# Optimization experiments

Hardware: AMD Instinct MI355X
Metric: run time of the kernel (lower is better)

Reference implementation:

```python
import jax, jax.numpy as jnp
import numpy as np

N = 1048576
NUM_POINTS = 9
L = 3
EPS = 1e-6
GMM_EPS = 1e-6  # diagonal regularizer used by the GaussianMixture fit


def _det2(m):
    return m[..., 0, 0] * m[..., 1, 1] - m[..., 0, 1] * m[..., 1, 0]


def _inv2(m, det):
    # closed-form 2x2 inverse via adjugate
    adj = jnp.stack([
        jnp.stack([m[..., 1, 1], -m[..., 0, 1]], axis=-1),
        jnp.stack([-m[..., 1, 0], m[..., 0, 0]], axis=-1),
    ], axis=-2)
    return adj / det[..., None, None]


def setup_inputs() -> dict:
    key = jax.random.key(0)
    k1, k2, k3, k4, k5, k6 = jax.random.split(key, 6)
    # ground-truth rotated rectangles -> 4 corners (N, 4, 2)
    center = jax.random.uniform(k1, (N, 2), jnp.float32, 0.0, 512.0)
    w = jax.random.uniform(k2, (N,), jnp.float32, 10.0, 60.0)
    h = jax.random.uniform(k3, (N,), jnp.float32, 10.0, 60.0)
    th = jax.random.uniform(k4, (N,), jnp.float32, 0.0, np.pi)
    c, s = jnp.cos(th), jnp.sin(th)
    # local corners ordered so edge 0->1 is the width axis, 1->2 the height axis
    lx = jnp.stack([-w, w, w, -w], axis=1) * 0.5  # (N,4)
    ly = jnp.stack([-h, -h, h, h], axis=1) * 0.5
    gx = c[:, None] * lx - s[:, None] * ly + center[:, 0:1]
    gy = s[:, None] * lx + c[:, None] * ly + center[:, 1:2]
    target = jnp.stack([gx, gy], axis=-1).astype(jnp.float32)  # (N,4,2)
    # predicted convex points scattered around the box center
    pred = center[:, None, :] + 5.0 * jax.random.normal(k5, (N, NUM_POINTS, 2), jnp.float32)
    return {"pred": pred, "target": target}


def reference(pred, target):
    pred = pred.reshape(-1, NUM_POINTS, 2)
    target = target.reshape(-1, 4, 2)
    # --- GMM fit (1 component) == closed-form MLE Gaussian ---
    p_mu = pred.mean(axis=1)                       # (N,2)
    xm = pred - p_mu[:, None, :]                   # (N,9,2)
    p_var = jnp.einsum('nki,nkj->nij', xm, xm) / NUM_POINTS \
        + GMM_EPS * jnp.eye(2, dtype=pred.dtype)   # (N,2,2)
    # --- gt2gaussian ---
    t_mu = target.mean(axis=1)                     # (N,2)
    e1 = target[:, 1, :] - target[:, 0, :]
    e2 = target[:, 2, :] - target[:, 1, :]
    w = jnp.sum(e1 * e1, axis=-1)                  # (N,)
    h = jnp.sum(e2 * e2, axis=-1)
    cs = e1 / jnp.sqrt(w)[:, None]                 # (cos, sin)
    c, s = cs[:, 0], cs[:, 1]
    R = jnp.stack([jnp.stack([c, -s], axis=-1),
                   jnp.stack([s, c], axis=-1)], axis=-2)  # (N,2,2)
    d = jnp.stack([w, h], axis=-1) / (4.0 * L * L)         # (N,2)
    t_var = jnp.einsum('nij,nj,nkj->nik', R, d, R)         # (N,2,2)
    # --- KLD(pred || target) with closed-form 2x2 inverse/det ---
    t_det = _det2(t_var)
    p_det = _det2(p_var)
    t_inv = _inv2(t_var, t_det)
    delta = p_mu - t_mu                            # (N,2)
    term1 = jnp.einsum('ni,nij,nj->n', delta, t_inv, delta)
    trace = jnp.einsum('nij,nji->n', t_inv, p_var)
    term2 = trace + jnp.log(t_det / p_det)
    kld = 0.5 * (term1 + term2) - 1.0
    kl_agg = jnp.maximum(kld, EPS)
    loss = 1.0 - 1.0 / (2.0 + jnp.sqrt(kl_agg))    # (N,)
    return loss.mean()  # loss_weight = 1.0, reduction = 'mean'
```

## Files before the change

kernel.cpp:

```cpp
#include <hip/hip_runtime.h>


__global__ __launch_bounds__(256) void kld_reppoints_kernel(
    const float* __restrict__ pred,
    const float* __restrict__ target,
    float* __restrict__ out,
    int n_total, float inv_n)
{
    __shared__ float sp[256 * 18];
    __shared__ float st[256 * 8];

    const int tid = threadIdx.x;
    const long long base = (long long)blockIdx.x * 256;
    const bool full = (base + 256 <= (long long)n_total);

    float px[9], py[9];
    float tx[4], ty[4];
    bool active = false;

    if (full) {
        const float4* gp = reinterpret_cast<const float4*>(pred + base * 18);
        float4* lp = reinterpret_cast<float4*>(sp);
        #pragma unroll
        for (int j = 0; j < 4; ++j) lp[tid + 256 * j] = gp[tid + 256 * j];
        if (tid < 128) lp[tid + 1024] = gp[tid + 1024];
        const float4* gt = reinterpret_cast<const float4*>(target + base * 8);
        float4* lt = reinterpret_cast<float4*>(st);
        lt[tid]       = gt[tid];
        lt[tid + 256] = gt[tid + 256];
        __syncthreads();

        const float2* mp = reinterpret_cast<const float2*>(sp) + tid * 9;
        #pragma unroll
        for (int k = 0; k < 9; ++k) { float2 v = mp[k]; px[k] = v.x; py[k] = v.y; }
        const float2* mt = reinterpret_cast<const float2*>(st) + tid * 4;
        #pragma unroll
        for (int k = 0; k < 4; ++k) { float2 v = mt[k]; tx[k] = v.x; ty[k] = v.y; }
        active = true;
    } else {
        long long n = base + tid;
        if (n < n_total) {
            const float2* p = reinterpret_cast<const float2*>(pred + n * 18);
            #pragma unroll
            for (int k = 0; k < 9; ++k) { float2 v = p[k]; px[k] = v.x; py[k] = v.y; }
            const float2* t = reinterpret_cast<const float2*>(target + n * 8);
            #pragma unroll
            for (int k = 0; k < 4; ++k) { float2 v = t[k]; tx[k] = v.x; ty[k] = v.y; }
            active = true;
        }
    }

    float loss = 0.0f;
    if (active) {
        const float inv9 = 1.0f / 9.0f;
        float sx = 0.f, sy = 0.f;
        #pragma unroll
        for (int k = 0; k < 9; ++k) { sx += px[k]; sy += py[k]; }
        float mux = sx * inv9, muy = sy * inv9;
        float a = 0.f, b = 0.f, d = 0.f;
        #pragma unroll
        for (int k = 0; k < 9; ++k) {
            float xx = px[k] - mux, yy = py[k] - muy;
            a += xx * xx; b += xx * yy; d += yy * yy;
        }
        a = a * inv9 + 1e-6f;
        b = b * inv9;
        d = d * inv9 + 1e-6f;

        float tmux = (tx[0] + tx[1] + tx[2] + tx[3]) * 0.25f;
        float tmuy = (ty[0] + ty[1] + ty[2] + ty[3]) * 0.25f;
        float e1x = tx[1] - tx[0], e1y = ty[1] - ty[0];
        float e2x = tx[2] - tx[1], e2y = ty[2] - ty[1];
        float w = e1x * e1x + e1y * e1y;
        float h = e2x * e2x + e2y * e2y;
        float sw = sqrtf(w);
        float c = e1x / sw, s = e1y / sw;
        const float invLL = 1.0f / 36.0f;
        float dw = w * invLL, dh = h * invLL;
        float tv00 = c * c * dw + s * s * dh;
        float tv01 = c * s * (dw - dh);
        float tv11 = s * s * dw + c * c * dh;

        float t_det = tv00 * tv11 - tv01 * tv01;
        float p_det = a * d - b * b;
        float inv_tdet = 1.0f / t_det;

        float dx = mux - tmux, dy = muy - tmuy;
        float term1 = (dx * dx * tv11 - 2.0f * dx * dy * tv01 + dy * dy * tv00) * inv_tdet;
        float trace = (tv11 * a - 2.0f * tv01 * b + tv00 * d) * inv_tdet;
        float term2 = trace + logf(t_det / p_det);
        float kld = 0.5f * (term1 + term2) - 1.0f;
        float kl = fmaxf(kld, 1e-6f);
        loss = 1.0f - 1.0f / (2.0f + sqrtf(kl));
    }

    #pragma unroll
    for (int off = 32; off > 0; off >>= 1)
        loss += __shfl_down(loss, off, 64);

    __shared__ float sm[4];
    int lane = tid & 63;
    int wid  = tid >> 6;
    __syncthreads();
    if (lane == 0) sm[wid] = loss;
    __syncthreads();
    if (tid == 0) {
        float tot = sm[0] + sm[1] + sm[2] + sm[3];
        atomicAdd(out, tot * inv_n);
    }
}

extern "C" void kernel_launch(void* const* d_in, const int* in_sizes, int n_in,
                              void* d_out, int out_size, void* d_ws, size_t ws_size,
                              hipStream_t stream) {
    const float* pred   = (const float*)d_in[0];
    const float* target = (const float*)d_in[1];
    float* out = (float*)d_out;

    int n = in_sizes[0] / 18;

    hipMemsetAsync(d_out, 0, (size_t)out_size * sizeof(float), stream);

    dim3 block(256);
    dim3 grid((n + 255) / 256);
    kld_reppoints_kernel<<<grid, block, 0, stream>>>(pred, target, out, n, 1.0f / (float)n);
}
```

Before: 164.9 us.

## Replace atomic reduction with two-pass partials and direct target float4 loads

Each block now writes its partial sum to workspace, and a second single-block kernel reduces the partials and scales by 1/n. This removes the memset launch and the 4096 same-address atomics. Target corners are now loaded straight from global memory as two float4s per thread instead of being staged through shared memory, which cuts LDS use and shared-memory traffic. The cost is an extra kernel launch plus a serial final kernel.

```diff
diff --git a/kernel.cpp b/kernel.cpp
--- a/kernel.cpp
+++ b/kernel.cpp
@@ -1,14 +1,13 @@
 #include <hip/hip_runtime.h>
 
 
-__global__ __launch_bounds__(256) void kld_reppoints_kernel(
+__global__ __launch_bounds__(256) void kld_partial_kernel(
     const float* __restrict__ pred,
     const float* __restrict__ target,
-    float* __restrict__ out,
-    int n_total, float inv_n)
+    float* __restrict__ ws,
+    int n_total)
 {
     __shared__ float sp[256 * 18];
-    __shared__ float st[256 * 8];
 
     const int tid = threadIdx.x;
     const long long base = (long long)blockIdx.x * 256;
@@ -24,18 +23,17 @@
         #pragma unroll
         for (int j = 0; j < 4; ++j) lp[tid + 256 * j] = gp[tid + 256 * j];
         if (tid < 128) lp[tid + 1024] = gp[tid + 1024];
-        const float4* gt = reinterpret_cast<const float4*>(target + base * 8);
-        float4* lt = reinterpret_cast<float4*>(st);
-        lt[tid]       = gt[tid];
-        lt[tid + 256] = gt[tid + 256];
+
+        const float4* gt = reinterpret_cast<const float4*>(target + base * 8) + tid * 2;
+        float4 ta = gt[0], tb = gt[1];
+        tx[0] = ta.x; ty[0] = ta.y; tx[1] = ta.z; ty[1] = ta.w;
+        tx[2] = tb.x; ty[2] = tb.y; tx[3] = tb.z; ty[3] = tb.w;
+
         __syncthreads();
 
         const float2* mp = reinterpret_cast<const float2*>(sp) + tid * 9;
         #pragma unroll
         for (int k = 0; k < 9; ++k) { float2 v = mp[k]; px[k] = v.x; py[k] = v.y; }
-        const float2* mt = reinterpret_cast<const float2*>(st) + tid * 4;
-        #pragma unroll
-        for (int k = 0; k < 4; ++k) { float2 v = mt[k]; tx[k] = v.x; ty[k] = v.y; }
         active = true;
     } else {
         long long n = base + tid;
@@ -104,10 +102,29 @@
     __syncthreads();
     if (lane == 0) sm[wid] = loss;
     __syncthreads();
-    if (tid == 0) {
-        float tot = sm[0] + sm[1] + sm[2] + sm[3];
-        atomicAdd(out, tot * inv_n);
-    }
+    if (tid == 0)
+        ws[blockIdx.x] = sm[0] + sm[1] + sm[2] + sm[3];
+}
+
+__global__ __launch_bounds__(256) void kld_final_kernel(
+    const float* __restrict__ ws, float* __restrict__ out,
+    int nblocks, float inv_n)
+{
+    float s = 0.0f;
+    for (int i = threadIdx.x; i < nblocks; i += 256)
+        s += ws[i];
+
+    #pragma unroll
+    for (int off = 32; off > 0; off >>= 1)
+        s += __shfl_down(s, off, 64);
+
+    __shared__ float sm[4];
+    int lane = threadIdx.x & 63;
+    int wid  = threadIdx.x >> 6;
+    if (lane == 0) sm[wid] = s;
+    __syncthreads();
+    if (threadIdx.x == 0)
+        out[0] = (sm[0] + sm[1] + sm[2] + sm[3]) * inv_n;
 }
 
 extern "C" void kernel_launch(void* const* d_in, const int* in_sizes, int n_in,
@@ -116,12 +133,11 @@
     const float* pred   = (const float*)d_in[0];
     const float* target = (const float*)d_in[1];
     float* out = (float*)d_out;
+    float* ws  = (float*)d_ws;
 
     int n = in_sizes[0] / 18;
+    int nblocks = (n + 255) / 256;
 
-    hipMemsetAsync(d_out, 0, (size_t)out_size * sizeof(float), stream);
-
-    dim3 block(256);
-    dim3 grid((n + 255) / 256);
-    kld_reppoints_kernel<<<grid, block, 0, stream>>>(pred, target, out, n, 1.0f / (float)n);
+    kld_partial_kernel<<<nblocks, 256, 0, stream>>>(pred, target, ws, n);
+    kld_final_kernel<<<1, 256, 0, stream>>>(ws, out, nblocks, 1.0f / (float)n);
 }
```

Result: faster. 138.7 us (-15.9%).
